# Optimization experiments

Hardware: AMD Instinct MI355X
Metric: run time of the kernel (lower is better)

## Reference

```python
import jax, jax.numpy as jnp
import numpy as np

N, E, A, D, B = 30000, 60000, 6, 16, 4096
F_IN, F_HID, F_EMB = 256, 256, 256
ALPHA = 0.2  # LeakyReLU negative slope


def _layer(node_embs, edge_embs, edge_list, node_list, Wn, We, ae, an, concat):
    out = Wn.shape[1]
    hn = node_embs @ Wn                      # [N, out]
    he = edge_embs @ We                      # [E, out]
    # stage 1: hyperedge update = attention over its member nodes
    gn = hn[edge_list]                       # [E, A, out] gather
    se = (he @ ae[:out])[:, None] + gn @ ae[out:]            # [E, A]
    att_e = jax.nn.softmax(jax.nn.leaky_relu(se, ALPHA), axis=1)
    new_edge = jnp.einsum('ea,eao->eo', att_e, gn)           # [E, out]
    # stage 2: node update = attention over its incident hyperedges
    ge = new_edge[node_list]                 # [N, D, out] gather
    sn = (hn @ an[:out])[:, None] + ge @ an[out:]            # [N, D]
    att_n = jax.nn.softmax(jax.nn.leaky_relu(sn, ALPHA), axis=1)
    new_node = jnp.einsum('nd,ndo->no', att_n, ge)           # [N, out]
    if concat:
        return jax.nn.elu(new_node), jax.nn.elu(new_edge)
    return new_node, new_edge


def setup_inputs() -> dict:
    key = jax.random.key(0)
    ks = jax.random.split(key, 16)
    s = 0.1
    return {
        'batch_inputs': jax.random.randint(ks[0], (B, A + 1), 0, N),
        'node_embs': jax.random.normal(ks[1], (N, F_IN), jnp.float32),
        'edge_embs': jax.random.normal(ks[2], (E, F_IN), jnp.float32),
        'edge_list': jax.random.randint(ks[3], (E, A), 0, N),
        'node_list': jax.random.randint(ks[4], (N, D), 0, E),
        'Wn1': jax.random.normal(ks[5], (F_IN, F_HID), jnp.float32) * s,
        'We1': jax.random.normal(ks[6], (F_IN, F_HID), jnp.float32) * s,
        'ae1': jax.random.normal(ks[7], (2 * F_HID,), jnp.float32) * s,
        'an1': jax.random.normal(ks[8], (2 * F_HID,), jnp.float32) * s,
        'Wn2': jax.random.normal(ks[9], (F_HID, F_EMB), jnp.float32) * s,
        'We2': jax.random.normal(ks[10], (F_HID, F_EMB), jnp.float32) * s,
        'ae2': jax.random.normal(ks[11], (2 * F_EMB,), jnp.float32) * s,
        'an2': jax.random.normal(ks[12], (2 * F_EMB,), jnp.float32) * s,
    }


def reference(batch_inputs, node_embs, edge_embs, edge_list, node_list,
              Wn1, We1, ae1, an1, Wn2, We2, ae2, an2):
    # single attention head (nheads=1), concat=True -> ELU; dropout identity (eval)
    n1, e1 = _layer(node_embs, edge_embs, edge_list, node_list, Wn1, We1, ae1, an1, True)
    n2, e2 = _layer(n1, e1, edge_list, node_list, Wn2, We2, ae2, an2, False)
    n2, e2 = jax.nn.elu(n2), jax.nn.elu(e2)
    # assemble: slot 0 = hyperedge embedding, slots 1..right-1 = node embeddings
    S = batch_inputs.shape[1]
    cols = jnp.arange(S - 1)
    nz = batch_inputs[:, :-1] != 0
    right = jnp.max(jnp.where(nz, cols, -1), axis=1) + 1      # [B]
    pos = jnp.arange(S)
    mask = (pos[None, :] >= 1) & (pos[None, :] < right[:, None])  # [B, S]
    gathered = n2[batch_inputs]                               # [B, S, F_EMB]
    out = jnp.where(mask[:, :, None], gathered, jnp.float32(0))
    out = out.at[:, 0, :].set(e2[batch_inputs[:, 0]])
    return out
```

## Files before the change

### kernel.cpp

```cpp
#include <hip/hip_runtime.h>
#include <stdint.h>

typedef unsigned short u16;
typedef unsigned int   u32;
typedef __attribute__((ext_vector_type(8))) short bf16x8;
typedef __attribute__((ext_vector_type(4))) float f32x4;

#define N_NODES 30000
#define N_EDGES 60000
#define A_DEG   6
#define D_DEG   16
#define BATCH   4096
#define FEAT    256
#define APAD    8

__device__ __forceinline__ float bfbits2f(u32 hi){ union{u32 u; float f;} v; v.u = hi; return v.f; }
__device__ __forceinline__ float bf2f(u16 h){ return bfbits2f(((u32)h)<<16); }
__device__ __forceinline__ u16 f2bf(float f){
  union{float f; u32 u;} v; v.f = f;
  u32 u = v.u;
  return (u16)((u + 0x7fffu + ((u>>16)&1u)) >> 16);
}

struct F4 { float x,y,z,w; };
struct F8 { float v[8]; };

__device__ __forceinline__ F4 load4(const float* p){
  float4 t = *reinterpret_cast<const float4*>(p);
  F4 f; f.x=t.x; f.y=t.y; f.z=t.z; f.w=t.w; return f;
}
__device__ __forceinline__ F4 load4(const u16* p){
  uint2 u = *reinterpret_cast<const uint2*>(p);
  F4 f;
  f.x = bfbits2f(u.x<<16);
  f.y = bfbits2f(u.x & 0xffff0000u);
  f.z = bfbits2f(u.y<<16);
  f.w = bfbits2f(u.y & 0xffff0000u);
  return f;
}
__device__ __forceinline__ F8 load8(const float* p){
  float4 a = *reinterpret_cast<const float4*>(p);
  float4 b = *reinterpret_cast<const float4*>(p+4);
  F8 f; f.v[0]=a.x; f.v[1]=a.y; f.v[2]=a.z; f.v[3]=a.w;
        f.v[4]=b.x; f.v[5]=b.y; f.v[6]=b.z; f.v[7]=b.w; return f;
}
__device__ __forceinline__ F8 load8(const u16* p){
  uint4 u = *reinterpret_cast<const uint4*>(p);
  F8 f;
  f.v[0]=bfbits2f(u.x<<16); f.v[1]=bfbits2f(u.x&0xffff0000u);
  f.v[2]=bfbits2f(u.y<<16); f.v[3]=bfbits2f(u.y&0xffff0000u);
  f.v[4]=bfbits2f(u.z<<16); f.v[5]=bfbits2f(u.z&0xffff0000u);
  f.v[6]=bfbits2f(u.w<<16); f.v[7]=bfbits2f(u.w&0xffff0000u);
  return f;
}
__device__ __forceinline__ void acc8(float* o, uint4 u, float ww){
  o[0] += ww*bfbits2f(u.x<<16); o[1] += ww*bfbits2f(u.x&0xffff0000u);
  o[2] += ww*bfbits2f(u.y<<16); o[3] += ww*bfbits2f(u.y&0xffff0000u);
  o[4] += ww*bfbits2f(u.z<<16); o[5] += ww*bfbits2f(u.z&0xffff0000u);
  o[6] += ww*bfbits2f(u.w<<16); o[7] += ww*bfbits2f(u.w&0xffff0000u);
}
__device__ __forceinline__ void store_bf8(u16* p, const float* f){
  uint4 u;
  u.x = (u32)f2bf(f[0]) | ((u32)f2bf(f[1])<<16);
  u.y = (u32)f2bf(f[2]) | ((u32)f2bf(f[3])<<16);
  u.z = (u32)f2bf(f[4]) | ((u32)f2bf(f[5])<<16);
  u.w = (u32)f2bf(f[6]) | ((u32)f2bf(f[7])<<16);
  *reinterpret_cast<uint4*>(p) = u;
}

__device__ __forceinline__ float eluf(float x){ return x > 0.f ? x : (__expf(x) - 1.f); }
__device__ __forceinline__ float lrelu(float x){ return x > 0.f ? x : 0.2f*x; }

__device__ __forceinline__ float wave_sum_lane0(float v){
  #pragma unroll
  for (int off = 32; off > 0; off >>= 1) v += __shfl_down(v, off, 64);
  return v;
}
__device__ __forceinline__ float half_sum_all(float v){
  #pragma unroll
  for (int off = 1; off < 32; off <<= 1) v += __shfl_xor(v, off, 64);
  return v;
}

__global__ __launch_bounds__(256) void wtrans_k(const float* __restrict__ W1,
    u16* __restrict__ Wt1, const float* __restrict__ W2, u16* __restrict__ Wt2)
{
  const float* W = blockIdx.z ? W2 : W1;
  u16* Wt        = blockIdx.z ? Wt2 : Wt1;
  __shared__ float T[32][33];
  const int bx = blockIdx.x;
  const int by = blockIdx.y;
  const int tc = threadIdx.x & 31;
  const int tr = threadIdx.x >> 5;
  #pragma unroll
  for (int i=0;i<4;i++){
    int r = tr + i*8;
    T[r][tc] = W[(bx*32 + r)*FEAT + by*32 + tc];
  }
  __syncthreads();
  #pragma unroll
  for (int i=0;i<4;i++){
    int r = tr + i*8;
    Wt[(by*32 + r)*FEAT + bx*32 + tc] = f2bf(T[tc][r]);
  }
}

__global__ __launch_bounds__(256) void wvec_k(
    const float* __restrict__ W1, const float* __restrict__ a1, float* __restrict__ o1,
    const float* __restrict__ W2, const float* __restrict__ a2, float* __restrict__ o2)
{
  const int sel  = blockIdx.x >> 6;
  const float* W = sel ? W2 : W1;
  const float* a = sel ? a2 : a1;
  float* o       = sel ? o2 : o1;
  const int lane = threadIdx.x & 63;
  const int row  = (blockIdx.x & 63)*4 + (threadIdx.x >> 6);
  const int c = lane*4;
  F4 h = load4(W + (long)row*FEAT + c);
  F4 v = load4(a + c);
  float p = wave_sum_lane0(h.x*v.x + h.y*v.y + h.z*v.z + h.w*v.w);
  if (lane == 0) o[row] = p;
}

template<bool ELU, typename TIN>
__global__ __launch_bounds__(256) void gemm_mfma_k(
    const TIN* __restrict__ X, const u16* __restrict__ Wt,
    const float* __restrict__ v1, const float* __restrict__ v2,
    u16* __restrict__ Y, float* __restrict__ hg, float* __restrict__ snb,
    int M)
{
  __shared__ u16 As[64][FEAT + APAD];
  __shared__ float hgs[64], sns[64];
  const int tid = threadIdx.x;
  const long row0 = (long)blockIdx.x * 64;

  if (tid < 64){ hgs[tid] = 0.f; sns[tid] = 0.f; }

  {
    const int c = (tid & 15) << 4;
    #pragma unroll
    for (int i=0;i<4;i++){
      const int r = (tid >> 4) + 16*i;
      u16* dst = &As[r][c];
      if (row0 + r < M){
        const TIN* src = X + (row0 + r)*FEAT + c;
        #pragma unroll
        for (int j=0;j<4;j++){
          F4 v = load4(src + 4*j);
          if (ELU){ v.x=eluf(v.x); v.y=eluf(v.y); v.z=eluf(v.z); v.w=eluf(v.w); }
          dst[4*j+0]=f2bf(v.x); dst[4*j+1]=f2bf(v.y);
          dst[4*j+2]=f2bf(v.z); dst[4*j+3]=f2bf(v.w);
        }
      } else {
        #pragma unroll
        for (int j=0;j<16;j++) dst[j] = 0;
      }
    }
  }
  __syncthreads();

  const int wave = tid >> 6;
  const int lane = tid & 63;
  const int l15  = lane & 15;
  const int kg   = lane >> 4;

  f32x4 acc[4][4] = {};

  for (int k0 = 0; k0 < FEAT; k0 += 32){
    bf16x8 a[4], b[4];
    #pragma unroll
    for (int rt=0;rt<4;rt++)
      a[rt] = *reinterpret_cast<const bf16x8*>(&As[rt*16 + l15][k0 + kg*8]);
    #pragma unroll
    for (int t=0;t<4;t++){
      const int n = wave*64 + t*16 + l15;
      b[t] = *reinterpret_cast<const bf16x8*>(Wt + (long)n*FEAT + k0 + kg*8);
    }
    #pragma unroll
    for (int rt=0;rt<4;rt++)
      #pragma unroll
      for (int t=0;t<4;t++)
        acc[rt][t] = __builtin_amdgcn_mfma_f32_16x16x32_bf16(a[rt], b[t], acc[rt][t], 0, 0, 0);
  }

  __syncthreads();

  float p1[4][4] = {}, p2[4][4] = {};
  #pragma unroll
  for (int t=0;t<4;t++){
    const int col = wave*64 + t*16 + l15;
    const float a1 = v1[col];
    const float a2 = v2[col];
    #pragma unroll
    for (int rt=0;rt<4;rt++){
      #pragma unroll
      for (int r=0;r<4;r++){
        const float val = acc[rt][t][r];
        As[rt*16 + kg*4 + r][col] = f2bf(val);
        p1[rt][r] += val * a1;
        p2[rt][r] += val * a2;
      }
    }
  }
  #pragma unroll
  for (int off=1; off<16; off<<=1){
    #pragma unroll
    for (int rt=0;rt<4;rt++)
      #pragma unroll
      for (int r=0;r<4;r++){
        p1[rt][r] += __shfl_xor(p1[rt][r], off, 64);
        p2[rt][r] += __shfl_xor(p2[rt][r], off, 64);
      }
  }
  if (l15 == 0){
    #pragma unroll
    for (int rt=0;rt<4;rt++)
      #pragma unroll
      for (int r=0;r<4;r++){
        atomicAdd(&hgs[rt*16 + kg*4 + r], p1[rt][r]);
        atomicAdd(&sns[rt*16 + kg*4 + r], p2[rt][r]);
      }
  }
  __syncthreads();

  {
    const int c = (tid & 15) << 4;
    #pragma unroll
    for (int i=0;i<4;i++){
      const int r = (tid >> 4) + 16*i;
      if (row0 + r < M){
        const uint4* s = reinterpret_cast<const uint4*>(&As[r][c]);
        uint4* d = reinterpret_cast<uint4*>(Y + (row0 + r)*FEAT + c);
        d[0] = s[0]; d[1] = s[1];
      }
    }
  }
  if (tid < 64 && row0 + tid < M){
    hg[row0 + tid]  = hgs[tid];
    snb[row0 + tid] = sns[tid];
  }
}

__global__ __launch_bounds__(256) void node_gemm_k(
    const u16* __restrict__ NE, const int* __restrict__ node_list,
    const float* __restrict__ snb1, const float* __restrict__ ned,
    const u16* __restrict__ Wt,
    const float* __restrict__ v1, const float* __restrict__ v2,
    u16* __restrict__ Y, float* __restrict__ hg, float* __restrict__ snb2,
    int M)
{
  __shared__ u16 As[64][FEAT + APAD];
  __shared__ float hgs[64], sns[64];
  const int tid = threadIdx.x;
  const long row0 = (long)blockIdx.x * 64;

  if (tid < 64){ hgs[tid] = 0.f; sns[tid] = 0.f; }

  const int hw = tid >> 5;
  const int hl = tid & 31;
  const int c  = hl*8;
  #pragma unroll
  for (int i=0;i<8;i++){
    const int r = hw*8 + i;
    const long n = row0 + r;
    u16* dst = &As[r][c];
    if (n < M){
      int idx[D_DEG];
      #pragma unroll
      for (int d=0; d<D_DEG; d++) idx[d] = node_list[n*D_DEG + d];
      float nv[D_DEG];
      #pragma unroll
      for (int d=0; d<D_DEG; d++) nv[d] = ned[idx[d]];
      const float sb = snb1[n];
      float w[D_DEG];
      float mx = -1e30f;
      #pragma unroll
      for (int d=0; d<D_DEG; d++){
        float s = lrelu(sb + nv[d]);
        w[d] = s; mx = fmaxf(mx, s);
      }
      float sum = 0.f;
      #pragma unroll
      for (int d=0; d<D_DEG; d++){ w[d] = __expf(w[d]-mx); sum += w[d]; }
      const float inv = 1.f/sum;

      uint4 hb[D_DEG];
      #pragma unroll
      for (int d=0; d<D_DEG; d++)
        hb[d] = *reinterpret_cast<const uint4*>(NE + (long)idx[d]*FEAT + c);
      float o[8] = {};
      #pragma unroll
      for (int d=0; d<D_DEG; d++) acc8(o, hb[d], w[d]*inv);

      #pragma unroll
      for (int j=0;j<8;j++) dst[j] = f2bf(eluf(o[j]));
    } else {
      #pragma unroll
      for (int j=0;j<8;j++) dst[j] = 0;
    }
  }
  __syncthreads();

  const int wave = tid >> 6;
  const int lane = tid & 63;
  const int l15  = lane & 15;
  const int kg   = lane >> 4;

  f32x4 acc[4][4] = {};

  for (int k0 = 0; k0 < FEAT; k0 += 32){
    bf16x8 a[4], b[4];
    #pragma unroll
    for (int rt=0;rt<4;rt++)
      a[rt] = *reinterpret_cast<const bf16x8*>(&As[rt*16 + l15][k0 + kg*8]);
    #pragma unroll
    for (int t=0;t<4;t++){
      const int n = wave*64 + t*16 + l15;
      b[t] = *reinterpret_cast<const bf16x8*>(Wt + (long)n*FEAT + k0 + kg*8);
    }
    #pragma unroll
    for (int rt=0;rt<4;rt++)
      #pragma unroll
      for (int t=0;t<4;t++)
        acc[rt][t] = __builtin_amdgcn_mfma_f32_16x16x32_bf16(a[rt], b[t], acc[rt][t], 0, 0, 0);
  }

  __syncthreads();

  float p1[4][4] = {}, p2[4][4] = {};
  #pragma unroll
  for (int t=0;t<4;t++){
    const int col = wave*64 + t*16 + l15;
    const float a1 = v1[col];
    const float a2 = v2[col];
    #pragma unroll
    for (int rt=0;rt<4;rt++){
      #pragma unroll
      for (int r=0;r<4;r++){
        const float val = acc[rt][t][r];
        As[rt*16 + kg*4 + r][col] = f2bf(val);
        p1[rt][r] += val * a1;
        p2[rt][r] += val * a2;
      }
    }
  }
  #pragma unroll
  for (int off=1; off<16; off<<=1){
    #pragma unroll
    for (int rt=0;rt<4;rt++)
      #pragma unroll
      for (int r=0;r<4;r++){
        p1[rt][r] += __shfl_xor(p1[rt][r], off, 64);
        p2[rt][r] += __shfl_xor(p2[rt][r], off, 64);
      }
  }
  if (l15 == 0){
    #pragma unroll
    for (int rt=0;rt<4;rt++)
      #pragma unroll
      for (int r=0;r<4;r++){
        atomicAdd(&hgs[rt*16 + kg*4 + r], p1[rt][r]);
        atomicAdd(&sns[rt*16 + kg*4 + r], p2[rt][r]);
      }
  }
  __syncthreads();

  {
    const int cc = (tid & 15) << 4;
    #pragma unroll
    for (int i=0;i<4;i++){
      const int r = (tid >> 4) + 16*i;
      if (row0 + r < M){
        const uint4* s = reinterpret_cast<const uint4*>(&As[r][cc]);
        uint4* d = reinterpret_cast<uint4*>(Y + (row0 + r)*FEAT + cc);
        d[0] = s[0]; d[1] = s[1];
      }
    }
  }
  if (tid < 64 && row0 + tid < M){
    hg[row0 + tid]   = hgs[tid];
    snb2[row0 + tid] = sns[tid];
  }
}

template<typename TIN, bool ELU>
__global__ __launch_bounds__(256) void edge_attn_k(const u16* __restrict__ Hn,
    const TIN* __restrict__ Xe, const float* __restrict__ wE,
    const int* __restrict__ edge_list,
    const float* __restrict__ hg, const float* __restrict__ an_hi,
    u16* __restrict__ NE, float* __restrict__ ned)
{
  const int tid = threadIdx.x;
  const int hl  = tid & 31;
  const int e   = blockIdx.x*8 + (tid >> 5);
  const int c   = hl*8;

  int idx[A_DEG];
  #pragma unroll
  for (int a=0;a<A_DEG;a++) idx[a] = edge_list[e*A_DEG + a];
  float hgv[A_DEG];
  #pragma unroll
  for (int a=0;a<A_DEG;a++) hgv[a] = hg[idx[a]];
  uint4 hb[A_DEG];
  #pragma unroll
  for (int a=0;a<A_DEG;a++)
    hb[a] = *reinterpret_cast<const uint4*>(Hn + (long)idx[a]*FEAT + c);

  float sb;
  {
    F8 x = load8(Xe + (long)e*FEAT + c);
    if (ELU){
      #pragma unroll
      for (int j=0;j<8;j++) x.v[j] = eluf(x.v[j]);
    }
    F8 v = load8(wE + c);
    float p = 0.f;
    #pragma unroll
    for (int j=0;j<8;j++) p += x.v[j]*v.v[j];
    sb = half_sum_all(p);
  }

  float w[A_DEG];
  float mx = -1e30f;
  #pragma unroll
  for (int a=0;a<A_DEG;a++){
    float s = lrelu(sb + hgv[a]);
    w[a] = s; mx = fmaxf(mx, s);
  }
  float sum = 0.f;
  #pragma unroll
  for (int a=0;a<A_DEG;a++){ w[a] = __expf(w[a]-mx); sum += w[a]; }
  const float inv = 1.f/sum;

  float o[8] = {};
  #pragma unroll
  for (int a=0;a<A_DEG;a++) acc8(o, hb[a], w[a]*inv);
  store_bf8(NE + (long)e*FEAT + c, o);

  F8 v = load8(an_hi + c);
  float p = 0.f;
  #pragma unroll
  for (int j=0;j<8;j++) p += o[j]*v.v[j];
  p = half_sum_all(p);
  if (hl == 0) ned[e] = p;
}

__global__ __launch_bounds__(256) void node_assemble_k(
    const u16* __restrict__ NE, const int* __restrict__ node_list,
    const float* __restrict__ snb, const float* __restrict__ ned,
    const int* __restrict__ batch, float* __restrict__ out)
{
  const int b   = blockIdx.x;
  const int tid = threadIdx.x;
  const int hw  = tid >> 5;
  const int hl  = tid & 31;
  const int c   = hl*8;

  int right = 0;
  #pragma unroll
  for (int cc=0; cc<6; cc++){ if (batch[b*7 + cc] != 0) right = cc+1; }

  if (hw == 6){
    const int e = batch[b*7 + 0];
    F8 x = load8(NE + (long)e*FEAT + c);
    float4 o0, o1;
    o0.x=eluf(x.v[0]); o0.y=eluf(x.v[1]); o0.z=eluf(x.v[2]); o0.w=eluf(x.v[3]);
    o1.x=eluf(x.v[4]); o1.y=eluf(x.v[5]); o1.z=eluf(x.v[6]); o1.w=eluf(x.v[7]);
    float* po = out + ((long)b*7 + 0)*FEAT + c;
    *reinterpret_cast<float4*>(po)   = o0;
    *reinterpret_cast<float4*>(po+4) = o1;
  } else if (hw < 6){
    const int s  = hw + 1;
    float* po = out + ((long)b*7 + s)*FEAT + c;
    if (s < right){
      const int n = batch[b*7 + s];
      int idx[D_DEG];
      #pragma unroll
      for (int d=0; d<D_DEG; d++) idx[d] = node_list[(long)n*D_DEG + d];
      float nv[D_DEG];
      #pragma unroll
      for (int d=0; d<D_DEG; d++) nv[d] = ned[idx[d]];
      const float sb = snb[n];
      float w[D_DEG];
      float mx = -1e30f;
      #pragma unroll
      for (int d=0; d<D_DEG; d++){
        float sc = lrelu(sb + nv[d]);
        w[d] = sc; mx = fmaxf(mx, sc);
      }
      float sum = 0.f;
      #pragma unroll
      for (int d=0; d<D_DEG; d++){ w[d] = __expf(w[d]-mx); sum += w[d]; }
      const float inv = 1.f/sum;

      uint4 hb[D_DEG];
      #pragma unroll
      for (int d=0; d<D_DEG; d++)
        hb[d] = *reinterpret_cast<const uint4*>(NE + (long)idx[d]*FEAT + c);
      float o[8] = {};
      #pragma unroll
      for (int d=0; d<D_DEG; d++) acc8(o, hb[d], w[d]*inv);

      float4 o0, o1;
      o0.x=eluf(o[0]); o0.y=eluf(o[1]); o0.z=eluf(o[2]); o0.w=eluf(o[3]);
      o1.x=eluf(o[4]); o1.y=eluf(o[5]); o1.z=eluf(o[6]); o1.w=eluf(o[7]);
      *reinterpret_cast<float4*>(po)   = o0;
      *reinterpret_cast<float4*>(po+4) = o1;
    } else {
      float4 z; z.x=0.f; z.y=0.f; z.z=0.f; z.w=0.f;
      *reinterpret_cast<float4*>(po)   = z;
      *reinterpret_cast<float4*>(po+4) = z;
    }
  }
}

extern "C" void kernel_launch(void* const* d_in, const int* in_sizes, int n_in,
                              void* d_out, int out_size, void* d_ws, size_t ws_size,
                              hipStream_t stream)
{
  const int*   batch      = (const int*)d_in[0];
  const float* node_embs  = (const float*)d_in[1];
  const float* edge_embs  = (const float*)d_in[2];
  const int*   edge_list  = (const int*)d_in[3];
  const int*   node_list  = (const int*)d_in[4];
  const float* Wn1 = (const float*)d_in[5];
  const float* We1 = (const float*)d_in[6];
  const float* ae1 = (const float*)d_in[7];
  const float* an1 = (const float*)d_in[8];
  const float* Wn2 = (const float*)d_in[9];
  const float* We2 = (const float*)d_in[10];
  const float* ae2 = (const float*)d_in[11];
  const float* an2 = (const float*)d_in[12];
  float* out = (float*)d_out;

  char* ws = (char*)d_ws;
  size_t off = 0;
  auto alloc = [&](size_t bytes)->void* {
    void* p = ws + off; off += (bytes + 255) & ~(size_t)255; return p;
  };
  u16* bHn = (u16*)alloc((size_t)N_NODES*FEAT*2);
  u16* bNE = (u16*)alloc((size_t)N_EDGES*FEAT*2);
  u16* Wt1 = (u16*)alloc((size_t)FEAT*FEAT*2);
  u16* Wt2 = (u16*)alloc((size_t)FEAT*FEAT*2);
  float* hg  = (float*)alloc((size_t)N_NODES*4);
  float* snb = (float*)alloc((size_t)N_NODES*4);
  float* ned = (float*)alloc((size_t)N_EDGES*4);
  float* wE1 = (float*)alloc(FEAT*4);
  float* wE2 = (float*)alloc(FEAT*4);

  dim3 blk(256);
  const int gemm_grid = (N_NODES + 63) / 64;

  wtrans_k<<<dim3(8,8,2), blk, 0, stream>>>(Wn1, Wt1, Wn2, Wt2);
  wvec_k<<<128, blk, 0, stream>>>(We1, ae1, wE1, We2, ae2, wE2);

  gemm_mfma_k<false,float><<<gemm_grid, blk, 0, stream>>>(node_embs, Wt1,
      ae1+FEAT, an1, bHn, hg, snb, N_NODES);
  edge_attn_k<float,false><<<N_EDGES/8, blk, 0, stream>>>(bHn, edge_embs, wE1,
      edge_list, hg, an1+FEAT, bNE, ned);

  node_gemm_k<<<gemm_grid, blk, 0, stream>>>(bNE, node_list, snb, ned,
      Wt2, ae2+FEAT, an2, bHn, hg, snb, N_NODES);

  edge_attn_k<u16,true><<<N_EDGES/8, blk, 0, stream>>>(bHn, bNE, wE2,
      edge_list, hg, an2+FEAT, bNE, ned);

  node_assemble_k<<<BATCH, blk, 0, stream>>>(bNE, node_list, snb, ned, batch, out);
}
```

Before: 288.0 us.

## Merge prep kernels, precompute layer-2 edge score, pair rows in node gather

Result: no change. 290.8 us (+1.0%).

```diff
diff --git a/kernel.cpp b/kernel.cpp
--- a/kernel.cpp
+++ b/kernel.cpp
@@ -82,44 +82,49 @@
   return v;
 }
 
-__global__ __launch_bounds__(256) void wtrans_k(const float* __restrict__ W1,
-    u16* __restrict__ Wt1, const float* __restrict__ W2, u16* __restrict__ Wt2)
+__global__ __launch_bounds__(256) void prep_k(
+    const float* __restrict__ Wn1, u16* __restrict__ Wt1,
+    const float* __restrict__ Wn2, u16* __restrict__ Wt2,
+    const float* __restrict__ We1, const float* __restrict__ ae1, float* __restrict__ wE1,
+    const float* __restrict__ We2, const float* __restrict__ ae2, float* __restrict__ wE2)
 {
-  const float* W = blockIdx.z ? W2 : W1;
-  u16* Wt        = blockIdx.z ? Wt2 : Wt1;
-  __shared__ float T[32][33];
-  const int bx = blockIdx.x;
-  const int by = blockIdx.y;
-  const int tc = threadIdx.x & 31;
-  const int tr = threadIdx.x >> 5;
-  #pragma unroll
-  for (int i=0;i<4;i++){
-    int r = tr + i*8;
-    T[r][tc] = W[(bx*32 + r)*FEAT + by*32 + tc];
-  }
-  __syncthreads();
-  #pragma unroll
-  for (int i=0;i<4;i++){
-    int r = tr + i*8;
-    Wt[(by*32 + r)*FEAT + bx*32 + tc] = f2bf(T[tc][r]);
-  }
-}
-
-__global__ __launch_bounds__(256) void wvec_k(
-    const float* __restrict__ W1, const float* __restrict__ a1, float* __restrict__ o1,
-    const float* __restrict__ W2, const float* __restrict__ a2, float* __restrict__ o2)
-{
-  const int sel  = blockIdx.x >> 6;
-  const float* W = sel ? W2 : W1;
-  const float* a = sel ? a2 : a1;
-  float* o       = sel ? o2 : o1;
-  const int lane = threadIdx.x & 63;
-  const int row  = (blockIdx.x & 63)*4 + (threadIdx.x >> 6);
-  const int c = lane*4;
-  F4 h = load4(W + (long)row*FEAT + c);
-  F4 v = load4(a + c);
-  float p = wave_sum_lane0(h.x*v.x + h.y*v.y + h.z*v.z + h.w*v.w);
-  if (lane == 0) o[row] = p;
+  if (blockIdx.z < 2){
+    const float* W = blockIdx.z ? Wn2 : Wn1;
+    u16* Wt        = blockIdx.z ? Wt2 : Wt1;
+    __shared__ float T[32][33];
+    const int bx = blockIdx.x;
+    const int by = blockIdx.y;
+    const int tc = threadIdx.x & 31;
+    const int tr = threadIdx.x >> 5;
+    #pragma unroll
+    for (int i=0;i<4;i++){
+      int r = tr + i*8;
+      T[r][tc] = W[(bx*32 + r)*FEAT + by*32 + tc];
+    }
+    __syncthreads();
+    #pragma unroll
+    for (int i=0;i<4;i++){
+      int r = tr + i*8;
+      Wt[(by*32 + r)*FEAT + bx*32 + tc] = f2bf(T[tc][r]);
+    }
+  } else {
+    const int vb   = blockIdx.y*8 + blockIdx.x;
+    const int lane = threadIdx.x & 63;
+    const int row  = vb*4 + (threadIdx.x >> 6);
+    const int c    = lane*4;
+    {
+      F4 h = load4(We1 + (long)row*FEAT + c);
+      F4 a = load4(ae1 + c);
+      float p = wave_sum_lane0(h.x*a.x + h.y*a.y + h.z*a.z + h.w*a.w);
+      if (lane == 0) wE1[row] = p;
+    }
+    {
+      F4 h = load4(We2 + (long)row*FEAT + c);
+      F4 a = load4(ae2 + c);
+      float p = wave_sum_lane0(h.x*a.x + h.y*a.y + h.z*a.z + h.w*a.w);
+      if (lane == 0) wE2[row] = p;
+    }
+  }
 }
 
 template<bool ELU, typename TIN>
@@ -259,44 +264,97 @@
   const int hw = tid >> 5;
   const int hl = tid & 31;
   const int c  = hl*8;
-  #pragma unroll
-  for (int i=0;i<8;i++){
-    const int r = hw*8 + i;
-    const long n = row0 + r;
-    u16* dst = &As[r][c];
-    if (n < M){
-      int idx[D_DEG];
-      #pragma unroll
-      for (int d=0; d<D_DEG; d++) idx[d] = node_list[n*D_DEG + d];
-      float nv[D_DEG];
-      #pragma unroll
-      for (int d=0; d<D_DEG; d++) nv[d] = ned[idx[d]];
-      const float sb = snb1[n];
-      float w[D_DEG];
-      float mx = -1e30f;
+  for (int i=0;i<4;i++){
+    const int rA = hw*8 + 2*i;
+    const int rB = rA + 1;
+    const long nA = row0 + rA;
+    const long nB = row0 + rB;
+    u16* dstA = &As[rA][c];
+    u16* dstB = &As[rB][c];
+    if (nB < M){
+      int idxA[D_DEG], idxB[D_DEG];
+      #pragma unroll
+      for (int d=0; d<D_DEG; d++) idxA[d] = node_list[nA*D_DEG + d];
+      #pragma unroll
+      for (int d=0; d<D_DEG; d++) idxB[d] = node_list[nB*D_DEG + d];
+      float nvA[D_DEG], nvB[D_DEG];
+      #pragma unroll
+      for (int d=0; d<D_DEG; d++) nvA[d] = ned[idxA[d]];
+      #pragma unroll
+      for (int d=0; d<D_DEG; d++) nvB[d] = ned[idxB[d]];
+      uint4 hbA[D_DEG], hbB[D_DEG];
+      #pragma unroll
+      for (int d=0; d<D_DEG; d++)
+        hbA[d] = *reinterpret_cast<const uint4*>(NE + (long)idxA[d]*FEAT + c);
+      #pragma unroll
+      for (int d=0; d<D_DEG; d++)
+        hbB[d] = *reinterpret_cast<const uint4*>(NE + (long)idxB[d]*FEAT + c);
+
+      const float sbA = snb1[nA];
+      const float sbB = snb1[nB];
+      float wA[D_DEG], wB[D_DEG];
+      float mxA = -1e30f, mxB = -1e30f;
       #pragma unroll
       for (int d=0; d<D_DEG; d++){
-        float s = lrelu(sb + nv[d]);
-        w[d] = s; mx = fmaxf(mx, s);
-      }
-      float sum = 0.f;
-      #pragma unroll
-      for (int d=0; d<D_DEG; d++){ w[d] = __expf(w[d]-mx); sum += w[d]; }
-      const float inv = 1.f/sum;
-
-      uint4 hb[D_DEG];
-      #pragma unroll
-      for (int d=0; d<D_DEG; d++)
-        hb[d] = *reinterpret_cast<const uint4*>(NE + (long)idx[d]*FEAT + c);
-      float o[8] = {};
-      #pragma unroll
-      for (int d=0; d<D_DEG; d++) acc8(o, hb[d], w[d]*inv);
-
-      #pragma unroll
-      for (int j=0;j<8;j++) dst[j] = f2bf(eluf(o[j]));
+        float sA = lrelu(sbA + nvA[d]); wA[d] = sA; mxA = fmaxf(mxA, sA);
+        float sB = lrelu(sbB + nvB[d]); wB[d] = sB; mxB = fmaxf(mxB, sB);
+      }
+      float sumA = 0.f, sumB = 0.f;
+      #pragma unroll
+      for (int d=0; d<D_DEG; d++){
+        wA[d] = __expf(wA[d]-mxA); sumA += wA[d];
+        wB[d] = __expf(wB[d]-mxB); sumB += wB[d];
+      }
+      const float invA = 1.f/sumA;
+      const float invB = 1.f/sumB;
+
+      float oA[8] = {};
+      #pragma unroll
+      for (int d=0; d<D_DEG; d++) acc8(oA, hbA[d], wA[d]*invA);
+      #pragma unroll
+      for (int j=0;j<8;j++) dstA[j] = f2bf(eluf(oA[j]));
+
+      float oB[8] = {};
+      #pragma unroll
+      for (int d=0; d<D_DEG; d++) acc8(oB, hbB[d], wB[d]*invB);
+      #pragma unroll
+      for (int j=0;j<8;j++) dstB[j] = f2bf(eluf(oB[j]));
     } else {
-      #pragma unroll
-      for (int j=0;j<8;j++) dst[j] = 0;
+      for (int t=0;t<2;t++){
+        const long n = (t==0) ? nA : nB;
+        u16* dst = (t==0) ? dstA : dstB;
+        if (n < M){
+          int idx[D_DEG];
+          #pragma unroll
+          for (int d=0; d<D_DEG; d++) idx[d] = node_list[n*D_DEG + d];
+          float nv[D_DEG];
+          #pragma unroll
+          for (int d=0; d<D_DEG; d++) nv[d] = ned[idx[d]];
+          uint4 hb[D_DEG];
+          #pragma unroll
+          for (int d=0; d<D_DEG; d++)
+            hb[d] = *reinterpret_cast<const uint4*>(NE + (long)idx[d]*FEAT + c);
+          const float sb = snb1[n];
+          float w[D_DEG];
+          float mx = -1e30f;
+          #pragma unroll
+          for (int d=0; d<D_DEG; d++){
+            float s = lrelu(sb + nv[d]); w[d] = s; mx = fmaxf(mx, s);
+          }
+          float sum = 0.f;
+          #pragma unroll
+          for (int d=0; d<D_DEG; d++){ w[d] = __expf(w[d]-mx); sum += w[d]; }
+          const float inv = 1.f/sum;
+          float o[8] = {};
+          #pragma unroll
+          for (int d=0; d<D_DEG; d++) acc8(o, hb[d], w[d]*inv);
+          #pragma unroll
+          for (int j=0;j<8;j++) dst[j] = f2bf(eluf(o[j]));
+        } else {
+          #pragma unroll
+          for (int j=0;j<8;j++) dst[j] = 0;
+        }
+      }
     }
   }
   __syncthreads();
@@ -383,11 +441,13 @@
   }
 }
 
-template<typename TIN, bool ELU>
+template<typename TIN, bool ELU, bool SB_PRE, bool SEB_OUT>
 __global__ __launch_bounds__(256) void edge_attn_k(const u16* __restrict__ Hn,
     const TIN* __restrict__ Xe, const float* __restrict__ wE,
     const int* __restrict__ edge_list,
     const float* __restrict__ hg, const float* __restrict__ an_hi,
+    const float* __restrict__ seb_in, const float* __restrict__ wE_nxt,
+    float* __restrict__ seb_out,
     u16* __restrict__ NE, float* __restrict__ ned)
 {
   const int tid = threadIdx.x;
@@ -407,7 +467,9 @@
     hb[a] = *reinterpret_cast<const uint4*>(Hn + (long)idx[a]*FEAT + c);
 
   float sb;
-  {
+  if (SB_PRE){
+    sb = seb_in[e];
+  } else {
     F8 x = load8(Xe + (long)e*FEAT + c);
     if (ELU){
       #pragma unroll
@@ -437,12 +499,22 @@
   for (int a=0;a<A_DEG;a++) acc8(o, hb[a], w[a]*inv);
   store_bf8(NE + (long)e*FEAT + c, o);
 
-  F8 v = load8(an_hi + c);
-  float p = 0.f;
-  #pragma unroll
-  for (int j=0;j<8;j++) p += o[j]*v.v[j];
-  p = half_sum_all(p);
-  if (hl == 0) ned[e] = p;
+  {
+    F8 v = load8(an_hi + c);
+    float p = 0.f;
+    #pragma unroll
+    for (int j=0;j<8;j++) p += o[j]*v.v[j];
+    p = half_sum_all(p);
+    if (hl == 0) ned[e] = p;
+  }
+  if (SEB_OUT){
+    F8 v = load8(wE_nxt + c);
+    float p = 0.f;
+    #pragma unroll
+    for (int j=0;j<8;j++) p += eluf(o[j])*v.v[j];
+    p = half_sum_all(p);
+    if (hl == 0) seb_out[e] = p;
+  }
 }
 
 __global__ __launch_bounds__(256) void node_assemble_k(
@@ -542,28 +614,29 @@
   u16* bNE = (u16*)alloc((size_t)N_EDGES*FEAT*2);
   u16* Wt1 = (u16*)alloc((size_t)FEAT*FEAT*2);
   u16* Wt2 = (u16*)alloc((size_t)FEAT*FEAT*2);
-  float* hg  = (float*)alloc((size_t)N_NODES*4);
-  float* snb = (float*)alloc((size_t)N_NODES*4);
-  float* ned = (float*)alloc((size_t)N_EDGES*4);
-  float* wE1 = (float*)alloc(FEAT*4);
-  float* wE2 = (float*)alloc(FEAT*4);
+  float* hg   = (float*)alloc((size_t)N_NODES*4);
+  float* snb  = (float*)alloc((size_t)N_NODES*4);
+  float* ned  = (float*)alloc((size_t)N_EDGES*4);
+  float* seb2 = (float*)alloc((size_t)N_EDGES*4);
+  float* wE1  = (float*)alloc(FEAT*4);
+  float* wE2  = (float*)alloc(FEAT*4);
 
   dim3 blk(256);
   const int gemm_grid = (N_NODES + 63) / 64;
 
-  wtrans_k<<<dim3(8,8,2), blk, 0, stream>>>(Wn1, Wt1, Wn2, Wt2);
-  wvec_k<<<128, blk, 0, stream>>>(We1, ae1, wE1, We2, ae2, wE2);
+  prep_k<<<dim3(8,8,3), blk, 0, stream>>>(Wn1, Wt1, Wn2, Wt2,
+      We1, ae1, wE1, We2, ae2, wE2);
 
   gemm_mfma_k<false,float><<<gemm_grid, blk, 0, stream>>>(node_embs, Wt1,
       ae1+FEAT, an1, bHn, hg, snb, N_NODES);
-  edge_attn_k<float,false><<<N_EDGES/8, blk, 0, stream>>>(bHn, edge_embs, wE1,
-      edge_list, hg, an1+FEAT, bNE, ned);
+  edge_attn_k<float,false,false,true><<<N_EDGES/8, blk, 0, stream>>>(bHn, edge_embs, wE1,
+      edge_list, hg, an1+FEAT, nullptr, wE2, seb2, bNE, ned);
 
   node_gemm_k<<<gemm_grid, blk, 0, stream>>>(bNE, node_list, snb, ned,
       Wt2, ae2+FEAT, an2, bHn, hg, snb, N_NODES);
 
-  edge_attn_k<u16,true><<<N_EDGES/8, blk, 0, stream>>>(bHn, bNE, wE2,
-      edge_list, hg, an2+FEAT, bNE, ned);
+  edge_attn_k<u16,true,true,false><<<N_EDGES/8, blk, 0, stream>>>(bHn, bNE, wE2,
+      edge_list, hg, an2+FEAT, seb2, nullptr, nullptr, bNE, ned);
 
   node_assemble_k<<<BATCH, blk, 0, stream>>>(bNE, node_list, snb, ned, batch, out);
 }
```
